# Optimization experiments

Measured on AMD Instinct MI355X. Metric: run time of the kernel, lower is better.

Reference implementation:

```python
import jax, jax.numpy as jnp
import numpy as np

B, CIN, H, W = 8, 32, 64, 64  # x1/x2 each 32 ch; concat -> 64
C = 2 * CIN


def setup_inputs() -> dict:
    key = jax.random.key(0)
    ks = jax.random.split(key, 8)
    s = 0.05
    return {
        "x1": jax.random.normal(ks[0], (B, CIN, H, W), jnp.float32),
        "x2": jax.random.normal(ks[1], (B, CIN, H, W), jnp.float32),
        "Wq": jax.random.normal(ks[2], (C // 2, C), jnp.float32) * s,
        "bq": jax.random.normal(ks[3], (C // 2,), jnp.float32) * s,
        "Wk": jax.random.normal(ks[4], (C // 2, C), jnp.float32) * s,
        "bk": jax.random.normal(ks[5], (C // 2,), jnp.float32) * s,
        "Wv": jax.random.normal(ks[6], (C, C), jnp.float32) * s,
        "Wsc": jax.random.normal(ks[7], (C // 2, C), jnp.float32) * s,
        "gamma": jnp.array([0.5], jnp.float32),
    }


def reference(x1, x2, Wq, bq, Wk, bk, Wv, Wsc, gamma):
    x = jnp.concatenate([x1, x2], axis=1)  # [b, c, h, w]
    b, c, h, w = x.shape
    hw = h * w
    # 1x1 convs == per-pixel linear projections
    q = (jnp.einsum('oc,bchw->bohw', Wq, x) + bq[None, :, None, None]).reshape(b, c // 2, hw)
    q = q.transpose(0, 2, 1)  # [b, hw, c/2]
    k = (jnp.einsum('oc,bchw->bohw', Wk, x) + bk[None, :, None, None]).reshape(b, c // 2, hw)
    am = jnp.einsum('bnd,bdm->bnm', q, k)  # [b, hw, hw]
    a = jax.nn.softmax(am, axis=1)  # softmax over dim=1 (queries axis) as in the torch code
    v = jnp.einsum('oc,bchw->bohw', Wv, x).reshape(b, c, hw)  # [b, c, hw]
    # out = bmm(v, a^T): out[b,c,n] = sum_m v[b,c,m] * a[b,n,m]
    out = jnp.einsum('bcm,bnm->bcn', v, a).reshape(b, c, h, w)
    out = gamma[0] * out + x
    out = jnp.einsum('oc,bchw->bohw', Wsc, out)  # [b, c/2, h, w]
    return out
```

## Files before the change

kernel.cpp:

```cpp
#include <hip/hip_runtime.h>

typedef __attribute__((ext_vector_type(8))) __bf16 bf16x8;
typedef __attribute__((ext_vector_type(4))) float f32x4;
typedef unsigned int uint32;

#define HW   4096
#define CCH  64
#define DQ   32
#define OC   32
#define LOG2E 1.4426950408889634f

#define WSV_OFF  0u
#define QB_OFF   2048u
#define KB_OFF   (QB_OFF + 524288u)
#define V2_OFF   (KB_OFF + 524288u)
#define XS_OFF   (V2_OFF + 1048576u)
#define ZP_OFF   (XS_OFF + 1048576u)
#define ZS_OFF   (ZP_OFF + 131072u)
#define VZB_OFF  (ZS_OFF + 32768u)
#define OUTP_OFF (VZB_OFF + 524288u)

__device__ __forceinline__ uint32 f2bf(float x) {
    uint32 u = __builtin_bit_cast(uint32, x);
    return (u + 0x7fffu + ((u >> 16) & 1u)) >> 16;
}
__device__ __forceinline__ uint32 packbf(float a, float b) {
    return f2bf(a) | (f2bf(b) << 16);
}
__device__ __forceinline__ bf16x8 ldfrag(const unsigned short* p) {
    union { uint4 u; bf16x8 f; } t;
    t.u = *(const uint4*)p;
    return t.f;
}
__device__ __forceinline__ float fexp2(float x) {
#if __has_builtin(__builtin_amdgcn_exp2f)
    return __builtin_amdgcn_exp2f(x);
#else
    return __expf(x * 0.6931471805599453f);
#endif
}

__global__ __launch_bounds__(256) void k_wcomb(const float* __restrict__ Wsc,
                                               const float* __restrict__ Wv,
                                               float* __restrict__ Wsv) {
    int t = blockIdx.x * 256 + threadIdx.x;
    if (t < OC * CCH) {
        int o = t / CCH, ci = t % CCH;
        float s = 0.f;
        #pragma unroll
        for (int c = 0; c < CCH; ++c) s += Wsc[o * CCH + c] * Wv[c * CCH + ci];
        Wsv[t] = s;
    }
}

__global__ __launch_bounds__(256) void k_proj(
    const float* __restrict__ x1, const float* __restrict__ x2,
    const float* __restrict__ Wq, const float* __restrict__ bq,
    const float* __restrict__ Wk, const float* __restrict__ bk,
    const float* __restrict__ Wsv, const float* __restrict__ Wsc,
    unsigned short* __restrict__ qb, unsigned short* __restrict__ kb,
    float* __restrict__ v2, float* __restrict__ xs) {
    __shared__ float wall[4 * DQ * CCH];
    __shared__ float bqs[DQ], bks[DQ];
    int t = threadIdx.x;
    for (int i = t; i < 4 * DQ * CCH; i += 256) {
        float v;
        if (i < 2048)      v = Wq[i];
        else if (i < 4096) v = Wk[i - 2048];
        else if (i < 6144) v = Wsv[i - 4096];
        else               v = Wsc[i - 6144];
        wall[i] = v;
    }
    if (t < DQ) { bqs[t] = bq[t]; bks[t] = bk[t]; }
    __syncthreads();

    int g = t >> 6, l = t & 63;
    int p = blockIdx.x * 64 + l;
    int b = p >> 12, n = p & 4095;
    const float* x1b = x1 + (size_t)b * 32 * HW;
    const float* x2b = x2 + (size_t)b * 32 * HW;
    float x[CCH];
    #pragma unroll
    for (int c = 0; c < 32; ++c) x[c] = x1b[c * HW + n];
    #pragma unroll
    for (int c = 0; c < 32; ++c) x[32 + c] = x2b[c * HW + n];

    const float* W = wall + g * (DQ * CCH);

    if (g < 2) {
        unsigned short* dst = (g == 0) ? qb : kb;
        const float* bias = (g == 0) ? bqs : bks;
        float scale = (g == 0) ? LOG2E : 1.0f;
        size_t row = ((size_t)b * HW + n) * DQ;
        for (int d0 = 0; d0 < DQ; d0 += 8) {
            float r[8];
            #pragma unroll
            for (int i = 0; i < 8; ++i) {
                int d = d0 + i;
                float a = bias[d];
                const float* wr = W + d * CCH;
                #pragma unroll
                for (int c = 0; c < CCH; ++c) a += wr[c] * x[c];
                r[i] = a * scale;
            }
            uint4 u;
            u.x = packbf(r[0], r[1]); u.y = packbf(r[2], r[3]);
            u.z = packbf(r[4], r[5]); u.w = packbf(r[6], r[7]);
            *(uint4*)(dst + row + d0) = u;
        }
    } else {
        float* dst = (g == 2) ? v2 : xs;
        for (int o = 0; o < OC; ++o) {
            float a = 0.f;
            const float* wr = W + o * CCH;
            #pragma unroll
            for (int c = 0; c < CCH; ++c) a += wr[c] * x[c];
            dst[((size_t)b * OC + o) * HW + n] = a;
        }
    }
}

__global__ __launch_bounds__(256, 4) void k_stats(
    const unsigned short* __restrict__ kb, const unsigned short* __restrict__ qb,
    float* __restrict__ zp) {
    int t = threadIdx.x;
    int w = t >> 6, l = t & 63;
    int lr = l & 15, lq = l >> 4;
    int bid = blockIdx.x;
    int nc = bid & 3, mg = (bid >> 2) & 31, b = bid >> 7;
    int m0 = mg * 128 + w * 32;

    const unsigned short* kbb = kb + ((size_t)b * HW) * DQ;
    bf16x8 af0 = ldfrag(kbb + (size_t)(m0 + lr) * DQ + lq * 8);
    bf16x8 af1 = ldfrag(kbb + (size_t)(m0 + 16 + lr) * DQ + lq * 8);
    const unsigned short* qp = qb + ((size_t)b * HW + nc * 1024 + lr) * DQ + lq * 8;

    f32x4 acc0 = {0.f, 0.f, 0.f, 0.f};
    f32x4 acc1 = {0.f, 0.f, 0.f, 0.f};
    f32x4 zz = {0.f, 0.f, 0.f, 0.f};
    #pragma unroll 4
    for (int i = 0; i < 64; ++i) {
        bf16x8 qf = ldfrag(qp);
        qp += 16 * DQ;
        f32x4 s0 = __builtin_amdgcn_mfma_f32_16x16x32_bf16(af0, qf, zz, 0, 0, 0);
        f32x4 s1 = __builtin_amdgcn_mfma_f32_16x16x32_bf16(af1, qf, zz, 0, 0, 0);
        acc0.x += fexp2(s0.x); acc0.y += fexp2(s0.y);
        acc0.z += fexp2(s0.z); acc0.w += fexp2(s0.w);
        acc1.x += fexp2(s1.x); acc1.y += fexp2(s1.y);
        acc1.z += fexp2(s1.z); acc1.w += fexp2(s1.w);
    }
    #pragma unroll
    for (int off = 1; off < 16; off <<= 1) {
        acc0.x += __shfl_xor(acc0.x, off); acc0.y += __shfl_xor(acc0.y, off);
        acc0.z += __shfl_xor(acc0.z, off); acc0.w += __shfl_xor(acc0.w, off);
        acc1.x += __shfl_xor(acc1.x, off); acc1.y += __shfl_xor(acc1.y, off);
        acc1.z += __shfl_xor(acc1.z, off); acc1.w += __shfl_xor(acc1.w, off);
    }
    if (lr == 0) {
        size_t base = (size_t)nc * 32768 + (size_t)b * HW;
        zp[base + m0 + lq * 4 + 0] = acc0.x;
        zp[base + m0 + lq * 4 + 1] = acc0.y;
        zp[base + m0 + lq * 4 + 2] = acc0.z;
        zp[base + m0 + lq * 4 + 3] = acc0.w;
        zp[base + m0 + 16 + lq * 4 + 0] = acc1.x;
        zp[base + m0 + 16 + lq * 4 + 1] = acc1.y;
        zp[base + m0 + 16 + lq * 4 + 2] = acc1.z;
        zp[base + m0 + 16 + lq * 4 + 3] = acc1.w;
    }
}

__global__ __launch_bounds__(256) void k_scale(const float* __restrict__ zp,
                                               const float* __restrict__ gamma,
                                               float* __restrict__ zs) {
    int i = (blockIdx.x * 256 + threadIdx.x) * 4;
    float4 a = *(const float4*)(zp + i);
    float4 b = *(const float4*)(zp + 32768 + i);
    float4 c = *(const float4*)(zp + 65536 + i);
    float4 d = *(const float4*)(zp + 98304 + i);
    float g = gamma[0];
    float4 r;
    r.x = g / (a.x + b.x + c.x + d.x);
    r.y = g / (a.y + b.y + c.y + d.y);
    r.z = g / (a.z + b.z + c.z + d.z);
    r.w = g / (a.w + b.w + c.w + d.w);
    *(float4*)(zs + i) = r;
}

__global__ __launch_bounds__(256) void k_vz(const float* __restrict__ v2,
                                            const float* __restrict__ zs,
                                            unsigned short* __restrict__ vzb) {
    int t = blockIdx.x * 256 + threadIdx.x;
    int e0 = t * 4;
    int b = e0 >> 17;
    int m = e0 & (HW - 1);
    float4 v = *(const float4*)(v2 + e0);
    float4 z = *(const float4*)(zs + (size_t)b * HW + m);
    uint2 r;
    r.x = packbf(v.x * z.x, v.y * z.y);
    r.y = packbf(v.z * z.z, v.w * z.w);
    *(uint2*)(vzb + e0) = r;
}

__global__ __launch_bounds__(256, 4) void k_attn(
    const unsigned short* __restrict__ qb, const unsigned short* __restrict__ kb,
    const unsigned short* __restrict__ vzb, float* __restrict__ outp) {
    __shared__ unsigned short fb[8192];
    int t = threadIdx.x;
    int w = t >> 6, l = t & 63;
    int lr = l & 15, lq = l >> 4;
    int bid = blockIdx.x;
    int mc = bid & 3, ng = (bid >> 2) & 31, b = bid >> 7;
    int nA = ng * 128 + w * 32;

    unsigned short* fbw = fb + w * 2048;
    int aw = (lr + ((lq >> 1) << 4)) * 8 + (lq & 1) * 4;

    bf16x8 qfA = ldfrag(qb + ((size_t)b * HW + nA + lr) * DQ + lq * 8);
    bf16x8 qfB = ldfrag(qb + ((size_t)b * HW + nA + 16 + lr) * DQ + lq * 8);
    const unsigned short* kp = kb + ((size_t)b * HW + lr) * DQ + lq * 8;
    const unsigned short* vp = vzb + ((size_t)b * OC + lr) * HW + lq * 8;

    f32x4 accA0 = {0.f,0.f,0.f,0.f}, accA1 = {0.f,0.f,0.f,0.f};
    f32x4 accB0 = {0.f,0.f,0.f,0.f}, accB1 = {0.f,0.f,0.f,0.f};
    f32x4 zz = {0.f,0.f,0.f,0.f};

    int mbeg = mc * 1024;
    for (int m0 = mbeg; m0 < mbeg + 1024; m0 += 64) {
        #pragma unroll
        for (int ph = 0; ph < 2; ++ph) {
            int mb = m0 + ph * 32;
            unsigned short* fA = fbw + ph * 512;
            unsigned short* fB = fbw + 1024 + ph * 512;
            bf16x8 a0  = ldfrag(kp + (size_t)mb * DQ);
            bf16x8 a1  = ldfrag(kp + (size_t)(mb + 16) * DQ);
            bf16x8 va0 = ldfrag(vp + mb);
            bf16x8 va1 = ldfrag(vp + 16 * HW + mb);
            f32x4 sA0 = __builtin_amdgcn_mfma_f32_16x16x32_bf16(a0, qfA, zz, 0, 0, 0);
            f32x4 sA1 = __builtin_amdgcn_mfma_f32_16x16x32_bf16(a1, qfA, zz, 0, 0, 0);
            f32x4 sB0 = __builtin_amdgcn_mfma_f32_16x16x32_bf16(a0, qfB, zz, 0, 0, 0);
            f32x4 sB1 = __builtin_amdgcn_mfma_f32_16x16x32_bf16(a1, qfB, zz, 0, 0, 0);
            uint2 pA0, pA1, pB0, pB1;
            pA0.x = packbf(fexp2(sA0.x), fexp2(sA0.y));
            pA0.y = packbf(fexp2(sA0.z), fexp2(sA0.w));
            pA1.x = packbf(fexp2(sA1.x), fexp2(sA1.y));
            pA1.y = packbf(fexp2(sA1.z), fexp2(sA1.w));
            pB0.x = packbf(fexp2(sB0.x), fexp2(sB0.y));
            pB0.y = packbf(fexp2(sB0.z), fexp2(sB0.w));
            pB1.x = packbf(fexp2(sB1.x), fexp2(sB1.y));
            pB1.y = packbf(fexp2(sB1.z), fexp2(sB1.w));
            *(uint2*)(fA + aw)       = pA0;
            *(uint2*)(fA + aw + 256) = pA1;
            *(uint2*)(fB + aw)       = pB0;
            *(uint2*)(fB + aw + 256) = pB1;
            bf16x8 pfA = ldfrag(fA + l * 8);
            bf16x8 pfB = ldfrag(fB + l * 8);
            accA0 = __builtin_amdgcn_mfma_f32_16x16x32_bf16(va0, pfA, accA0, 0, 0, 0);
            accA1 = __builtin_amdgcn_mfma_f32_16x16x32_bf16(va1, pfA, accA1, 0, 0, 0);
            accB0 = __builtin_amdgcn_mfma_f32_16x16x32_bf16(va0, pfB, accB0, 0, 0, 0);
            accB1 = __builtin_amdgcn_mfma_f32_16x16x32_bf16(va1, pfB, accB1, 0, 0, 0);
        }
    }

    int n_A = nA + lr, n_B = nA + 16 + lr;
    size_t obase = ((size_t)mc * 8 + b) * OC * HW;
    #pragma unroll
    for (int r = 0; r < 4; ++r) {
        int o0 = lq * 4 + r;
        outp[obase + (size_t)o0 * HW + n_A]        = accA0[r];
        outp[obase + (size_t)(o0 + 16) * HW + n_A] = accA1[r];
        outp[obase + (size_t)o0 * HW + n_B]        = accB0[r];
        outp[obase + (size_t)(o0 + 16) * HW + n_B] = accB1[r];
    }
}

__global__ __launch_bounds__(256) void k_red(const float* __restrict__ outp,
                                             const float* __restrict__ xs,
                                             float* __restrict__ out) {
    int i = (blockIdx.x * 256 + threadIdx.x) * 4;
    float4 a = *(const float4*)(outp + i);
    float4 b = *(const float4*)(outp + 1048576 + i);
    float4 c = *(const float4*)(outp + 2097152 + i);
    float4 d = *(const float4*)(outp + 3145728 + i);
    float4 x = *(const float4*)(xs + i);
    float4 r;
    r.x = a.x + b.x + c.x + d.x + x.x;
    r.y = a.y + b.y + c.y + d.y + x.y;
    r.z = a.z + b.z + c.z + d.z + x.z;
    r.w = a.w + b.w + c.w + d.w + x.w;
    *(float4*)(out + i) = r;
}

extern "C" void kernel_launch(void* const* d_in, const int* in_sizes, int n_in,
                              void* d_out, int out_size, void* d_ws, size_t ws_size,
                              hipStream_t stream) {
    const float* x1    = (const float*)d_in[0];
    const float* x2    = (const float*)d_in[1];
    const float* Wq    = (const float*)d_in[2];
    const float* bq    = (const float*)d_in[3];
    const float* Wk    = (const float*)d_in[4];
    const float* bk    = (const float*)d_in[5];
    const float* Wv    = (const float*)d_in[6];
    const float* Wsc   = (const float*)d_in[7];
    const float* gamma = (const float*)d_in[8];
    float* out = (float*)d_out;
    float* ws  = (float*)d_ws;

    float*          wsv  = ws + WSV_OFF;
    unsigned short* qbp  = (unsigned short*)(ws + QB_OFF);
    unsigned short* kbp  = (unsigned short*)(ws + KB_OFF);
    float*          v2   = ws + V2_OFF;
    float*          xsp  = ws + XS_OFF;
    float*          zpp  = ws + ZP_OFF;
    float*          zsp  = ws + ZS_OFF;
    unsigned short* vzb  = (unsigned short*)(ws + VZB_OFF);
    float*          outp = ws + OUTP_OFF;

    k_wcomb<<<8, 256, 0, stream>>>(Wsc, Wv, wsv);
    k_proj<<<512, 256, 0, stream>>>(x1, x2, Wq, bq, Wk, bk, wsv, Wsc,
                                    qbp, kbp, v2, xsp);
    k_stats<<<1024, 256, 0, stream>>>(kbp, qbp, zpp);
    k_scale<<<32, 256, 0, stream>>>(zpp, gamma, zsp);
    k_vz<<<1024, 256, 0, stream>>>(v2, zsp, vzb);
    k_attn<<<1024, 256, 0, stream>>>(qbp, kbp, vzb, outp);
    k_red<<<1024, 256, 0, stream>>>(outp, xsp, out);
}
```

Before: 179.2 us.

## Split attention and stats over 8 chunks, fuse scale kernels, store partials in bf16

The key/query reductions in k_stats and k_attn are split into 8 chunks instead of 4, which doubles the grid to 2048 blocks. The block index is reordered so the batch index varies fastest, and both kernels get a higher occupancy bound. k_scale and k_vz are fused into one k_zvz kernel. k_attn writes its partial outputs as bf16 rather than fp32 to halve the traffic into k_red, and the P-matrix packing now truncates via a perm instruction instead of rounding. k_proj drops its shared-memory weight staging and reads weights directly with a wave-uniform branch. The bf16 partials and the truncation both add rounding error, and the fused k_zvz launches only 128 blocks.

```diff
diff --git a/kernel.cpp b/kernel.cpp
--- a/kernel.cpp
+++ b/kernel.cpp
@@ -13,11 +13,10 @@
 #define WSV_OFF  0u
 #define QB_OFF   2048u
 #define KB_OFF   (QB_OFF + 524288u)
-#define V2_OFF   (KB_OFF + 524288u)
-#define XS_OFF   (V2_OFF + 1048576u)
-#define ZP_OFF   (XS_OFF + 1048576u)
-#define ZS_OFF   (ZP_OFF + 131072u)
-#define VZB_OFF  (ZS_OFF + 32768u)
+#define XS_OFF   (KB_OFF + 524288u)
+#define V2_OFF   (XS_OFF + 1048576u)
+#define ZP_OFF   (V2_OFF + 1048576u)
+#define VZB_OFF  (ZP_OFF + 262144u)
 #define OUTP_OFF (VZB_OFF + 524288u)
 
 __device__ __forceinline__ uint32 f2bf(float x) {
@@ -26,6 +25,10 @@
 }
 __device__ __forceinline__ uint32 packbf(float a, float b) {
     return f2bf(a) | (f2bf(b) << 16);
+}
+__device__ __forceinline__ uint32 packbf_t(float a, float b) {
+    return __builtin_amdgcn_perm(__builtin_bit_cast(uint32, b),
+                                 __builtin_bit_cast(uint32, a), 0x07060302u);
 }
 __device__ __forceinline__ bf16x8 ldfrag(const unsigned short* p) {
     union { uint4 u; bf16x8 f; } t;
@@ -60,45 +63,31 @@
     const float* __restrict__ Wsv, const float* __restrict__ Wsc,
     unsigned short* __restrict__ qb, unsigned short* __restrict__ kb,
     float* __restrict__ v2, float* __restrict__ xs) {
-    __shared__ float wall[4 * DQ * CCH];
-    __shared__ float bqs[DQ], bks[DQ];
     int t = threadIdx.x;
-    for (int i = t; i < 4 * DQ * CCH; i += 256) {
-        float v;
-        if (i < 2048)      v = Wq[i];
-        else if (i < 4096) v = Wk[i - 2048];
-        else if (i < 6144) v = Wsv[i - 4096];
-        else               v = Wsc[i - 6144];
-        wall[i] = v;
-    }
-    if (t < DQ) { bqs[t] = bq[t]; bks[t] = bk[t]; }
-    __syncthreads();
-
-    int g = t >> 6, l = t & 63;
+    int g = __builtin_amdgcn_readfirstlane(t >> 6);
+    int l = t & 63;
     int p = blockIdx.x * 64 + l;
     int b = p >> 12, n = p & 4095;
-    const float* x1b = x1 + (size_t)b * 32 * HW;
-    const float* x2b = x2 + (size_t)b * 32 * HW;
+    const float* x1b = x1 + (size_t)b * 32 * HW + n;
+    const float* x2b = x2 + (size_t)b * 32 * HW + n;
     float x[CCH];
     #pragma unroll
-    for (int c = 0; c < 32; ++c) x[c] = x1b[c * HW + n];
-    #pragma unroll
-    for (int c = 0; c < 32; ++c) x[32 + c] = x2b[c * HW + n];
-
-    const float* W = wall + g * (DQ * CCH);
+    for (int c = 0; c < 32; ++c) x[c] = x1b[(size_t)c * HW];
+    #pragma unroll
+    for (int c = 0; c < 32; ++c) x[32 + c] = x2b[(size_t)c * HW];
 
     if (g < 2) {
-        unsigned short* dst = (g == 0) ? qb : kb;
-        const float* bias = (g == 0) ? bqs : bks;
-        float scale = (g == 0) ? LOG2E : 1.0f;
+        const float* W    = g ? Wk : Wq;
+        const float* bias = g ? bk : bq;
+        float scale = g ? 1.0f : LOG2E;
+        unsigned short* dst = g ? kb : qb;
         size_t row = ((size_t)b * HW + n) * DQ;
         for (int d0 = 0; d0 < DQ; d0 += 8) {
             float r[8];
             #pragma unroll
             for (int i = 0; i < 8; ++i) {
-                int d = d0 + i;
-                float a = bias[d];
-                const float* wr = W + d * CCH;
+                const float* wr = W + (d0 + i) * CCH;
+                float a = bias[d0 + i];
                 #pragma unroll
                 for (int c = 0; c < CCH; ++c) a += wr[c] * x[c];
                 r[i] = a * scale;
@@ -109,10 +98,11 @@
             *(uint4*)(dst + row + d0) = u;
         }
     } else {
-        float* dst = (g == 2) ? v2 : xs;
+        const float* W = (g == 2) ? Wsv : Wsc;
+        float* dst     = (g == 2) ? v2  : xs;
         for (int o = 0; o < OC; ++o) {
+            const float* wr = W + o * CCH;
             float a = 0.f;
-            const float* wr = W + o * CCH;
             #pragma unroll
             for (int c = 0; c < CCH; ++c) a += wr[c] * x[c];
             dst[((size_t)b * OC + o) * HW + n] = a;
@@ -120,26 +110,26 @@
     }
 }
 
-__global__ __launch_bounds__(256, 4) void k_stats(
+__global__ __launch_bounds__(256, 8) void k_stats(
     const unsigned short* __restrict__ kb, const unsigned short* __restrict__ qb,
     float* __restrict__ zp) {
     int t = threadIdx.x;
     int w = t >> 6, l = t & 63;
     int lr = l & 15, lq = l >> 4;
     int bid = blockIdx.x;
-    int nc = bid & 3, mg = (bid >> 2) & 31, b = bid >> 7;
+    int b = bid & 7, nc = (bid >> 3) & 7, mg = bid >> 6;
     int m0 = mg * 128 + w * 32;
 
     const unsigned short* kbb = kb + ((size_t)b * HW) * DQ;
     bf16x8 af0 = ldfrag(kbb + (size_t)(m0 + lr) * DQ + lq * 8);
     bf16x8 af1 = ldfrag(kbb + (size_t)(m0 + 16 + lr) * DQ + lq * 8);
-    const unsigned short* qp = qb + ((size_t)b * HW + nc * 1024 + lr) * DQ + lq * 8;
+    const unsigned short* qp = qb + ((size_t)b * HW + nc * 512 + lr) * DQ + lq * 8;
 
     f32x4 acc0 = {0.f, 0.f, 0.f, 0.f};
     f32x4 acc1 = {0.f, 0.f, 0.f, 0.f};
     f32x4 zz = {0.f, 0.f, 0.f, 0.f};
     #pragma unroll 4
-    for (int i = 0; i < 64; ++i) {
+    for (int i = 0; i < 32; ++i) {
         bf16x8 qf = ldfrag(qp);
         qp += 16 * DQ;
         f32x4 s0 = __builtin_amdgcn_mfma_f32_16x16x32_bf16(af0, qf, zz, 0, 0, 0);
@@ -169,47 +159,33 @@
     }
 }
 
-__global__ __launch_bounds__(256) void k_scale(const float* __restrict__ zp,
-                                               const float* __restrict__ gamma,
-                                               float* __restrict__ zs) {
-    int i = (blockIdx.x * 256 + threadIdx.x) * 4;
-    float4 a = *(const float4*)(zp + i);
-    float4 b = *(const float4*)(zp + 32768 + i);
-    float4 c = *(const float4*)(zp + 65536 + i);
-    float4 d = *(const float4*)(zp + 98304 + i);
-    float g = gamma[0];
-    float4 r;
-    r.x = g / (a.x + b.x + c.x + d.x);
-    r.y = g / (a.y + b.y + c.y + d.y);
-    r.z = g / (a.z + b.z + c.z + d.z);
-    r.w = g / (a.w + b.w + c.w + d.w);
-    *(float4*)(zs + i) = r;
-}
-
-__global__ __launch_bounds__(256) void k_vz(const float* __restrict__ v2,
-                                            const float* __restrict__ zs,
-                                            unsigned short* __restrict__ vzb) {
-    int t = blockIdx.x * 256 + threadIdx.x;
-    int e0 = t * 4;
-    int b = e0 >> 17;
-    int m = e0 & (HW - 1);
-    float4 v = *(const float4*)(v2 + e0);
-    float4 z = *(const float4*)(zs + (size_t)b * HW + m);
-    uint2 r;
-    r.x = packbf(v.x * z.x, v.y * z.y);
-    r.y = packbf(v.z * z.z, v.w * z.w);
-    *(uint2*)(vzb + e0) = r;
-}
-
-__global__ __launch_bounds__(256, 4) void k_attn(
+__global__ __launch_bounds__(256) void k_zvz(const float* __restrict__ zp,
+                                             const float* __restrict__ v2,
+                                             const float* __restrict__ gamma,
+                                             unsigned short* __restrict__ vzb) {
+    int i = blockIdx.x * 256 + threadIdx.x;
+    float s = 0.f;
+    #pragma unroll
+    for (int nc = 0; nc < 8; ++nc) s += zp[nc * 32768 + i];
+    float zs = gamma[0] / s;
+    int b = i >> 12, m = i & 4095;
+    const float* vsrc = v2 + ((size_t)b * OC) * HW + m;
+    unsigned short* dst = vzb + ((size_t)b * OC) * HW + m;
+    #pragma unroll 8
+    for (int o = 0; o < OC; ++o) {
+        dst[(size_t)o * HW] = (unsigned short)f2bf(vsrc[(size_t)o * HW] * zs);
+    }
+}
+
+__global__ __launch_bounds__(256, 8) void k_attn(
     const unsigned short* __restrict__ qb, const unsigned short* __restrict__ kb,
-    const unsigned short* __restrict__ vzb, float* __restrict__ outp) {
+    const unsigned short* __restrict__ vzb, unsigned short* __restrict__ outp) {
     __shared__ unsigned short fb[8192];
     int t = threadIdx.x;
     int w = t >> 6, l = t & 63;
     int lr = l & 15, lq = l >> 4;
     int bid = blockIdx.x;
-    int mc = bid & 3, ng = (bid >> 2) & 31, b = bid >> 7;
+    int b = bid & 7, mc = (bid >> 3) & 7, ng = bid >> 6;
     int nA = ng * 128 + w * 32;
 
     unsigned short* fbw = fb + w * 2048;
@@ -224,8 +200,8 @@
     f32x4 accB0 = {0.f,0.f,0.f,0.f}, accB1 = {0.f,0.f,0.f,0.f};
     f32x4 zz = {0.f,0.f,0.f,0.f};
 
-    int mbeg = mc * 1024;
-    for (int m0 = mbeg; m0 < mbeg + 1024; m0 += 64) {
+    int mbeg = mc * 512;
+    for (int m0 = mbeg; m0 < mbeg + 512; m0 += 64) {
         #pragma unroll
         for (int ph = 0; ph < 2; ++ph) {
             int mb = m0 + ph * 32;
@@ -240,14 +216,14 @@
             f32x4 sB0 = __builtin_amdgcn_mfma_f32_16x16x32_bf16(a0, qfB, zz, 0, 0, 0);
             f32x4 sB1 = __builtin_amdgcn_mfma_f32_16x16x32_bf16(a1, qfB, zz, 0, 0, 0);
             uint2 pA0, pA1, pB0, pB1;
-            pA0.x = packbf(fexp2(sA0.x), fexp2(sA0.y));
-            pA0.y = packbf(fexp2(sA0.z), fexp2(sA0.w));
-            pA1.x = packbf(fexp2(sA1.x), fexp2(sA1.y));
-            pA1.y = packbf(fexp2(sA1.z), fexp2(sA1.w));
-            pB0.x = packbf(fexp2(sB0.x), fexp2(sB0.y));
-            pB0.y = packbf(fexp2(sB0.z), fexp2(sB0.w));
-            pB1.x = packbf(fexp2(sB1.x), fexp2(sB1.y));
-            pB1.y = packbf(fexp2(sB1.z), fexp2(sB1.w));
+            pA0.x = packbf_t(fexp2(sA0.x), fexp2(sA0.y));
+            pA0.y = packbf_t(fexp2(sA0.z), fexp2(sA0.w));
+            pA1.x = packbf_t(fexp2(sA1.x), fexp2(sA1.y));
+            pA1.y = packbf_t(fexp2(sA1.z), fexp2(sA1.w));
+            pB0.x = packbf_t(fexp2(sB0.x), fexp2(sB0.y));
+            pB0.y = packbf_t(fexp2(sB0.z), fexp2(sB0.w));
+            pB1.x = packbf_t(fexp2(sB1.x), fexp2(sB1.y));
+            pB1.y = packbf_t(fexp2(sB1.z), fexp2(sB1.w));
             *(uint2*)(fA + aw)       = pA0;
             *(uint2*)(fA + aw + 256) = pA1;
             *(uint2*)(fB + aw)       = pB0;
@@ -262,31 +238,31 @@
     }
 
     int n_A = nA + lr, n_B = nA + 16 + lr;
-    size_t obase = ((size_t)mc * 8 + b) * OC * HW;
+    unsigned short* ob = outp + ((size_t)(mc * 8 + b) * OC) * HW;
     #pragma unroll
     for (int r = 0; r < 4; ++r) {
         int o0 = lq * 4 + r;
-        outp[obase + (size_t)o0 * HW + n_A]        = accA0[r];
-        outp[obase + (size_t)(o0 + 16) * HW + n_A] = accA1[r];
-        outp[obase + (size_t)o0 * HW + n_B]        = accB0[r];
-        outp[obase + (size_t)(o0 + 16) * HW + n_B] = accB1[r];
-    }
-}
-
-__global__ __launch_bounds__(256) void k_red(const float* __restrict__ outp,
+        ob[(size_t)o0 * HW + n_A]        = (unsigned short)f2bf(accA0[r]);
+        ob[(size_t)(o0 + 16) * HW + n_A] = (unsigned short)f2bf(accA1[r]);
+        ob[(size_t)o0 * HW + n_B]        = (unsigned short)f2bf(accB0[r]);
+        ob[(size_t)(o0 + 16) * HW + n_B] = (unsigned short)f2bf(accB1[r]);
+    }
+}
+
+__global__ __launch_bounds__(256) void k_red(const unsigned short* __restrict__ outp,
                                              const float* __restrict__ xs,
                                              float* __restrict__ out) {
     int i = (blockIdx.x * 256 + threadIdx.x) * 4;
-    float4 a = *(const float4*)(outp + i);
-    float4 b = *(const float4*)(outp + 1048576 + i);
-    float4 c = *(const float4*)(outp + 2097152 + i);
-    float4 d = *(const float4*)(outp + 3145728 + i);
-    float4 x = *(const float4*)(xs + i);
-    float4 r;
-    r.x = a.x + b.x + c.x + d.x + x.x;
-    r.y = a.y + b.y + c.y + d.y + x.y;
-    r.z = a.z + b.z + c.z + d.z + x.z;
-    r.w = a.w + b.w + c.w + d.w + x.w;
+    float4 r = *(const float4*)(xs + i);
+    const unsigned short* op = outp + i;
+    #pragma unroll
+    for (int mc = 0; mc < 8; ++mc) {
+        uint2 p = *(const uint2*)(op + (size_t)mc * 1048576);
+        r.x += __builtin_bit_cast(float, p.x << 16);
+        r.y += __builtin_bit_cast(float, p.x & 0xffff0000u);
+        r.z += __builtin_bit_cast(float, p.y << 16);
+        r.w += __builtin_bit_cast(float, p.y & 0xffff0000u);
+    }
     *(float4*)(out + i) = r;
 }
 
@@ -308,19 +284,17 @@
     float*          wsv  = ws + WSV_OFF;
     unsigned short* qbp  = (unsigned short*)(ws + QB_OFF);
     unsigned short* kbp  = (unsigned short*)(ws + KB_OFF);
+    float*          xsp  = ws + XS_OFF;
     float*          v2   = ws + V2_OFF;
-    float*          xsp  = ws + XS_OFF;
     float*          zpp  = ws + ZP_OFF;
-    float*          zsp  = ws + ZS_OFF;
     unsigned short* vzb  = (unsigned short*)(ws + VZB_OFF);
-    float*          outp = ws + OUTP_OFF;
+    unsigned short* outp = (unsigned short*)(ws + OUTP_OFF);
 
     k_wcomb<<<8, 256, 0, stream>>>(Wsc, Wv, wsv);
     k_proj<<<512, 256, 0, stream>>>(x1, x2, Wq, bq, Wk, bk, wsv, Wsc,
                                     qbp, kbp, v2, xsp);
-    k_stats<<<1024, 256, 0, stream>>>(kbp, qbp, zpp);
-    k_scale<<<32, 256, 0, stream>>>(zpp, gamma, zsp);
-    k_vz<<<1024, 256, 0, stream>>>(v2, zsp, vzb);
-    k_attn<<<1024, 256, 0, stream>>>(qbp, kbp, vzb, outp);
+    k_stats<<<2048, 256, 0, stream>>>(kbp, qbp, zpp);
+    k_zvz<<<128, 256, 0, stream>>>(zpp, v2, gamma, vzb);
+    k_attn<<<2048, 256, 0, stream>>>(qbp, kbp, vzb, outp);
     k_red<<<1024, 256, 0, stream>>>(outp, xsp, out);
 }
```

Result: no change. 179.5 us (+0.2%).
